# Optimization experiments

Measured on AMD Instinct MI355X. Metric: run time of the kernel, lower is better.

The kernel has to match this reference:

```python
import jax, jax.numpy as jnp
import numpy as np

# Object condensation loss config (matches init_kwargs / HGCalML defaults)
Q_MIN = 0.5
S_B = 1.0
POT_SCALE = 1.0
REP_SCALE = 1.0
BETA_SCALE = 1.0
E_WEIGHT = 1.0
HUBER_DELTA = 2.0
E_DEN_OFFSET = 1.0
K_MAX = 192          # object-id slots per event; id 0 = noise
EPS = 1e-6

B, N = 4, 50000


def setup_inputs() -> dict:
    key = jax.random.key(0)
    k1, k2, k3, k4, k5 = jax.random.split(key, 5)
    return {
        "beta": jax.random.uniform(k1, (B, N, 1), dtype=jnp.float32),
        "ccoords": jax.random.normal(k2, (B, N, 2), dtype=jnp.float32),
        "pred_energy": jax.random.uniform(k3, (B, N, 1), dtype=jnp.float32),
        "true_energy": jax.random.uniform(k4, (B, N, 1), dtype=jnp.float32),
        "truth_idx": jax.random.randint(k5, (B, N), 0, K_MAX, dtype=jnp.int32),
    }


def _per_event(beta, ccoords, pred_e, true_e, tidx):
    # beta: [N,1], ccoords: [N,2], tidx: [N] int (0 = noise)
    beta = jnp.clip(beta[:, 0], 1e-4, 1.0 - 1e-4)            # [N]
    q = jnp.arctanh(beta) ** 2 + Q_MIN                        # charge  [N]

    ids = jnp.arange(K_MAX)
    M = (tidx[:, None] == ids[None, :]) & (ids[None, :] > 0)  # [N,K] membership
    Mf = M.astype(q.dtype)
    obj_valid = jnp.any(M, axis=0)                            # [K]
    vf = obj_valid.astype(q.dtype)

    # condensation point alpha_k = argmax_q over members of object k
    qM = jnp.where(M, q[:, None], -1.0)                       # [N,K]
    idx_alpha = jnp.argmax(qM, axis=0)                        # [K]
    x_alpha = ccoords[idx_alpha]                              # [K,2]
    q_alpha = q[idx_alpha]                                    # [K]
    beta_alpha = beta[idx_alpha]                              # [K]

    # pairwise hit<->condensation-point distances
    d2 = jnp.sum((ccoords[:, None, :] - x_alpha[None, :, :]) ** 2, axis=-1)  # [N,K]

    # attractive potential (members), repulsive hinge (non-members of valid objects)
    att = jnp.sum(d2 * q_alpha[None, :] * Mf, axis=-1)                       # [N]
    dist = jnp.sqrt(d2 + EPS)
    rep = jnp.sum(jnp.maximum(0.0, 1.0 - dist) * q_alpha[None, :]
                  * (1.0 - Mf) * vf[None, :], axis=-1)                       # [N]
    L_V = jnp.mean(q * (POT_SCALE * att + REP_SCALE * rep))

    n_obj = jnp.sum(vf) + EPS
    L_beta = BETA_SCALE * jnp.sum((1.0 - beta_alpha) * vf) / n_obj

    noise = (tidx == 0).astype(q.dtype)
    L_noise = S_B * jnp.sum(beta * noise) / (jnp.sum(noise) + EPS)

    # energy payload loss: relative error, Huber, beta-weighted per object
    ediff = (pred_e[:, 0] - true_e[:, 0]) / (true_e[:, 0] + E_DEN_OFFSET)
    ad = jnp.abs(ediff)
    eh = jnp.where(ad <= HUBER_DELTA, 0.5 * ad ** 2,
                   HUBER_DELTA * (ad - 0.5 * HUBER_DELTA))                   # [N]
    pw = Mf * beta[:, None]                                                  # [N,K]
    per_obj_e = jnp.sum(pw * eh[:, None], axis=0) / (jnp.sum(pw, axis=0) + EPS)
    L_E = E_WEIGHT * jnp.sum(per_obj_e * vf) / n_obj

    return L_V + L_beta + L_noise + L_E


def reference(beta, ccoords, pred_energy, true_energy, truth_idx):
    per_ev = jax.vmap(_per_event)(beta, ccoords, pred_energy, true_energy, truth_idx)
    return jnp.mean(per_ev)
```

## Files before the change

### kernel.cpp

```cpp
#include <hip/hip_runtime.h>
#include <math.h>

#define KM 192
#define EPSF 1e-6f
#define QMIN 0.5f
#define BLKA 256
#define HA 4
#define TILEA (BLKA * HA)
#define BLKM 512

__device__ __forceinline__ float clipb(float b) {
    return fminf(fmaxf(b, 1e-4f), 1.0f - 1e-4f);
}
__device__ __forceinline__ float fast_atanh(float b) {
    float r = (1.f + b) * __builtin_amdgcn_rcpf(1.f - b);
    return 0.34657359f * __builtin_amdgcn_logf(r);
}

__global__ void __launch_bounds__(BLKA)
k_amax(const float* __restrict__ beta, const int* __restrict__ tidx,
       unsigned long long* __restrict__ pscr, int N, int HBT) {
    const int e = blockIdx.y;
    __shared__ unsigned long long smax[KM];
    for (int k = threadIdx.x; k < KM; k += BLKA) smax[k] = 0ull;
    __syncthreads();
    const size_t base = (size_t)e * N;
    #pragma unroll
    for (int h = 0; h < HA; ++h) {
        int i = blockIdx.x * TILEA + h * BLKA + threadIdx.x;
        if (i < N) {
            int t = tidx[base + i];
            if (t > 0) {
                float bc = clipb(beta[base + i]);
                unsigned long long pack =
                    ((unsigned long long)__float_as_uint(bc) << 32) |
                    (unsigned long long)(unsigned)(N - 1 - i);
                atomicMax(&smax[t], pack);
            }
        }
    }
    __syncthreads();
    unsigned long long* row = pscr + ((size_t)e * HBT + blockIdx.x) * KM;
    for (int k = threadIdx.x; k < KM; k += BLKA) row[k] = smax[k];
}

__global__ void __launch_bounds__(256)
k_alpha(const unsigned long long* __restrict__ pscr, const float* __restrict__ cc,
        float4* __restrict__ alpha, float* __restrict__ abw,
        float* __restrict__ enm, float* __restrict__ eden,
        float* __restrict__ scal, unsigned int* __restrict__ cnt,
        int N, int HBT) {
    const int e = blockIdx.x;
    const int k = threadIdx.x;
    if (k < KM) {
        const unsigned long long* pk = pscr + (size_t)e * HBT * KM + k;
        unsigned long long v = 0ull;
        #pragma unroll 8
        for (int t = 0; t < HBT; ++t) {
            unsigned long long p = pk[(size_t)t * KM];
            if (p > v) v = p;
        }
        float4 a = make_float4(0.f, 0.f, 0.f, EPSF);
        float bw = 0.f;
        if (v) {
            int idx = N - 1 - (int)(unsigned)(v & 0xffffffffull);
            bw = __uint_as_float((unsigned)(v >> 32));
            float at = fast_atanh(bw);
            float2 cp = ((const float2*)cc)[(size_t)e * N + idx];
            a.x = cp.x; a.y = cp.y;
            a.z = fmaf(at, at, QMIN);
            a.w = fmaf(cp.x, cp.x, fmaf(cp.y, cp.y, EPSF));
        }
        alpha[e * KM + k] = a;
        abw  [e * KM + k] = bw;
    }
    for (int z = threadIdx.x; z < KM; z += 256) {
        enm [e * KM + z] = 0.f;
        eden[e * KM + z] = 0.f;
    }
    if (threadIdx.x < 8) scal[e * 8 + threadIdx.x] = 0.f;
    if (blockIdx.x == 0 && threadIdx.x == 0) cnt[0] = 0u;
}

__global__ void __launch_bounds__(BLKM)
k_main(const float* __restrict__ beta, const float* __restrict__ cc,
       const float* __restrict__ pe,   const float* __restrict__ te,
       const int* __restrict__ tidx,   const float4* __restrict__ alpha,
       const float* __restrict__ abw,
       float* __restrict__ enm, float* __restrict__ eden,
       float* __restrict__ scal, unsigned int* __restrict__ cnt,
       float* __restrict__ out, int N, int B) {
    const int e = blockIdx.y;
    __shared__ float sn[KM], sd[KM];
    __shared__ float sw[24];
    __shared__ int   lastFlag;
    for (int k = threadIdx.x; k < KM; k += BLKM) { sn[k] = 0.f; sd[k] = 0.f; }
    __syncthreads();

    const size_t base = (size_t)e * N;
    const int i = blockIdx.x * BLKM + threadIdx.x;
    const bool ok = i < N;
    const size_t ii = base + (ok ? i : 0);
    float2 cp = ((const float2*)cc)[ii];
    float  bc = clipb(beta[ii]);
    int    t  = ok ? tidx[ii] : 0;
    float  at = fast_atanh(bc);
    float  qq = ok ? fmaf(at, at, QMIN) : 0.f;
    float  pp = fmaf(cp.x, cp.x, cp.y * cp.y);

    const float4* __restrict__ ae = alpha + e * KM;
    float r0 = 0.f, r1 = 0.f, r2 = 0.f, r3 = 0.f;
    for (int k = 0; k < KM; k += 4) {
        float4 a0 = ae[k], a1 = ae[k + 1], a2 = ae[k + 2], a3 = ae[k + 3];
        float d0 = fmaf(-2.f, fmaf(cp.x, a0.x, cp.y * a0.y), pp + a0.w);
        float d1 = fmaf(-2.f, fmaf(cp.x, a1.x, cp.y * a1.y), pp + a1.w);
        float d2 = fmaf(-2.f, fmaf(cp.x, a2.x, cp.y * a2.y), pp + a2.w);
        float d3 = fmaf(-2.f, fmaf(cp.x, a3.x, cp.y * a3.y), pp + a3.w);
        r0 = fmaf(fmaxf(1.f - __builtin_amdgcn_sqrtf(d0), 0.f), a0.z, r0);
        r1 = fmaf(fmaxf(1.f - __builtin_amdgcn_sqrtf(d1), 0.f), a1.z, r1);
        r2 = fmaf(fmaxf(1.f - __builtin_amdgcn_sqrtf(d2), 0.f), a2.z, r2);
        r3 = fmaf(fmaxf(1.f - __builtin_amdgcn_sqrtf(d3), 0.f), a3.z, r3);
    }
    float rep = (r0 + r1) + (r2 + r3);
    float att = 0.f, lv = 0.f, bn = 0.f, cn = 0.f;

    if (t > 0) {
        float4 av = ae[t];
        float dx = cp.x - av.x, dy = cp.y - av.y;
        float d2 = fmaf(dx, dx, dy * dy);
        att = d2 * av.z;
        rep -= fmaxf(1.f - __builtin_amdgcn_sqrtf(d2 + EPSF), 0.f) * av.z;
        float tev = te[ii];
        float edv = (pe[ii] - tev) * __builtin_amdgcn_rcpf(tev + 1.f);
        float ad  = fabsf(edv);
        float eh  = (ad <= 2.f) ? 0.5f * ad * ad : 2.f * (ad - 1.f);
        atomicAdd(&sn[t], bc * eh);
        atomicAdd(&sd[t], bc);
    } else if (ok) { bn = bc; cn = 1.f; }
    lv = qq * (att + rep);
    __syncthreads();

    if (threadIdx.x < KM) {
        float vd = sd[threadIdx.x];
        if (vd != 0.f) {
            atomicAdd(&enm [e * KM + threadIdx.x], sn[threadIdx.x]);
            atomicAdd(&eden[e * KM + threadIdx.x], vd);
        }
    }
    for (int off = 32; off > 0; off >>= 1) {
        lv += __shfl_down(lv, off);
        bn += __shfl_down(bn, off);
        cn += __shfl_down(cn, off);
    }
    const int wid = threadIdx.x >> 6;
    if ((threadIdx.x & 63) == 0) { sw[wid] = lv; sw[8 + wid] = bn; sw[16 + wid] = cn; }
    __syncthreads();
    if (threadIdx.x == 0) {
        float a = 0.f, b2 = 0.f, c2 = 0.f;
        #pragma unroll
        for (int w = 0; w < 8; ++w) { a += sw[w]; b2 += sw[8 + w]; c2 += sw[16 + w]; }
        atomicAdd(&scal[e * 8 + 0], a);
        atomicAdd(&scal[e * 8 + 3], b2);
        atomicAdd(&scal[e * 8 + 4], c2);
    }

    if (threadIdx.x == 0) {
        __threadfence();
        unsigned int old = atomicAdd(cnt, 1u);
        lastFlag = (old == gridDim.x * gridDim.y - 1u);
    }
    __syncthreads();
    if (!lastFlag) return;
    __threadfence();

    volatile float* ven = enm;
    volatile float* ved = eden;
    volatile float* vsc = scal;
    float tot = 0.f;
    for (int ev = 0; ev < B; ++ev) {
        float lb = 0.f, nv = 0.f, le = 0.f;
        if (threadIdx.x < KM) {
            float bw = abw[ev * KM + threadIdx.x];
            if (bw > 0.f) {
                lb = 1.f - bw;
                nv = 1.f;
                le = ven[ev * KM + threadIdx.x] / (ved[ev * KM + threadIdx.x] + EPSF);
            }
        }
        for (int off = 32; off > 0; off >>= 1) {
            lb += __shfl_down(lb, off);
            nv += __shfl_down(nv, off);
            le += __shfl_down(le, off);
        }
        if ((threadIdx.x & 63) == 0) { sw[wid] = lb; sw[8 + wid] = nv; sw[16 + wid] = le; }
        __syncthreads();
        if (threadIdx.x == 0) {
            float lbs = 0.f, nvs = 0.f, les = 0.f;
            #pragma unroll
            for (int w = 0; w < 8; ++w) { lbs += sw[w]; nvs += sw[8 + w]; les += sw[16 + w]; }
            float nobj = nvs + EPSF;
            tot += vsc[ev * 8 + 0] / (float)N + lbs / nobj
                 + vsc[ev * 8 + 3] / (vsc[ev * 8 + 4] + EPSF) + les / nobj;
        }
        __syncthreads();
    }
    if (threadIdx.x == 0) out[0] = tot / (float)B;
}

extern "C" void kernel_launch(void* const* d_in, const int* in_sizes, int n_in,
                              void* d_out, int out_size, void* d_ws, size_t ws_size,
                              hipStream_t stream) {
    const int B = 4;
    const int N = in_sizes[0] / B;
    const int HBT = (N + TILEA - 1) / TILEA;
    const int MB  = (N + BLKM - 1) / BLKM;

    const float* beta = (const float*)d_in[0];
    const float* cc   = (const float*)d_in[1];
    const float* pe   = (const float*)d_in[2];
    const float* te   = (const float*)d_in[3];
    const int*   tidx = (const int*)  d_in[4];
    float* out = (float*)d_out;

    char* ws = (char*)d_ws;
    unsigned long long* pscr = (unsigned long long*)ws;
    float4* alpha = (float4*)(ws + (size_t)B * HBT * KM * 8);
    float*  abw   = (float*)(alpha + B * KM);
    float*  enm   = abw  + B * KM;
    float*  eden  = enm  + B * KM;
    float*  scal  = eden + B * KM;
    unsigned int* cnt = (unsigned int*)(scal + B * 8);

    k_amax<<<dim3(HBT, B), dim3(BLKA), 0, stream>>>(beta, tidx, pscr, N, HBT);
    k_alpha<<<dim3(B), dim3(256), 0, stream>>>(pscr, cc, alpha, abw, enm, eden, scal, cnt, N, HBT);
    k_main<<<dim3(MB, B), dim3(BLKM), 0, stream>>>(
        beta, cc, pe, te, tidx, alpha, abw, enm, eden, scal, cnt, out, N, B);
}
```

Baseline: 98.99 us.

## Fuse argmax reduction via global atomics and last-block finalize, pack alphas in LDS

Merges the per-tile argmax scratch pass and the separate alpha-gather kernel into one kernel. Each block folds its maxima into global packed slots with atomicMax, and the last block to finish builds a SoA-packed alpha table. k_main now stages that table in shared memory and computes distances directly as dx²+dy² instead of the expanded form. Block size drops to 256. Workspace zeroing moves to a hipMemsetAsync, so there are still three stream operations but one fewer kernel and less scratch traffic; the cost is more global atomics from many more blocks.

```diff
diff --git a/kernel.cpp b/kernel.cpp
--- a/kernel.cpp
+++ b/kernel.cpp
@@ -2,12 +2,10 @@
 #include <math.h>
 
 #define KM 192
+#define KG 48
 #define EPSF 1e-6f
 #define QMIN 0.5f
-#define BLKA 256
-#define HA 4
-#define TILEA (BLKA * HA)
-#define BLKM 512
+#define BLK 256
 
 __device__ __forceinline__ float clipb(float b) {
     return fminf(fmaxf(b, 1e-4f), 1.0f - 1e-4f);
@@ -17,119 +15,122 @@
     return 0.34657359f * __builtin_amdgcn_logf(r);
 }
 
-__global__ void __launch_bounds__(BLKA)
+__global__ void __launch_bounds__(BLK)
 k_amax(const float* __restrict__ beta, const int* __restrict__ tidx,
-       unsigned long long* __restrict__ pscr, int N, int HBT) {
+       const float* __restrict__ cc,
+       unsigned long long* __restrict__ packs,
+       float* __restrict__ pkf, float* __restrict__ abw,
+       unsigned int* __restrict__ cnt, int N, int B) {
     const int e = blockIdx.y;
     __shared__ unsigned long long smax[KM];
-    for (int k = threadIdx.x; k < KM; k += BLKA) smax[k] = 0ull;
-    __syncthreads();
-    const size_t base = (size_t)e * N;
-    #pragma unroll
-    for (int h = 0; h < HA; ++h) {
-        int i = blockIdx.x * TILEA + h * BLKA + threadIdx.x;
-        if (i < N) {
-            int t = tidx[base + i];
-            if (t > 0) {
-                float bc = clipb(beta[base + i]);
-                unsigned long long pack =
-                    ((unsigned long long)__float_as_uint(bc) << 32) |
-                    (unsigned long long)(unsigned)(N - 1 - i);
-                atomicMax(&smax[t], pack);
-            }
-        }
-    }
-    __syncthreads();
-    unsigned long long* row = pscr + ((size_t)e * HBT + blockIdx.x) * KM;
-    for (int k = threadIdx.x; k < KM; k += BLKA) row[k] = smax[k];
-}
-
-__global__ void __launch_bounds__(256)
-k_alpha(const unsigned long long* __restrict__ pscr, const float* __restrict__ cc,
-        float4* __restrict__ alpha, float* __restrict__ abw,
-        float* __restrict__ enm, float* __restrict__ eden,
-        float* __restrict__ scal, unsigned int* __restrict__ cnt,
-        int N, int HBT) {
-    const int e = blockIdx.x;
-    const int k = threadIdx.x;
-    if (k < KM) {
-        const unsigned long long* pk = pscr + (size_t)e * HBT * KM + k;
-        unsigned long long v = 0ull;
-        #pragma unroll 8
-        for (int t = 0; t < HBT; ++t) {
-            unsigned long long p = pk[(size_t)t * KM];
-            if (p > v) v = p;
-        }
-        float4 a = make_float4(0.f, 0.f, 0.f, EPSF);
-        float bw = 0.f;
+    __shared__ int lastFlag;
+    if (threadIdx.x < KM) smax[threadIdx.x] = 0ull;
+    __syncthreads();
+    const int i = blockIdx.x * BLK + threadIdx.x;
+    if (i < N) {
+        int t = tidx[(size_t)e * N + i];
+        if (t > 0) {
+            float bc = clipb(beta[(size_t)e * N + i]);
+            unsigned long long pack =
+                ((unsigned long long)__float_as_uint(bc) << 32) |
+                (unsigned long long)(unsigned)(N - 1 - i);
+            atomicMax(&smax[t], pack);
+        }
+    }
+    __syncthreads();
+    if (threadIdx.x < KM) {
+        unsigned long long v = smax[threadIdx.x];
+        if (v) atomicMax(&packs[e * KM + threadIdx.x], v);
+    }
+
+    if (threadIdx.x == 0) {
+        __threadfence();
+        unsigned int old = atomicAdd(&cnt[0], 1u);
+        lastFlag = (old == gridDim.x * gridDim.y - 1u);
+    }
+    __syncthreads();
+    if (!lastFlag) return;
+
+    for (int s = threadIdx.x; s < B * KM; s += BLK) {
+        unsigned long long v = atomicMax(&packs[s], 0ull);
+        int e2 = s / KM, k = s - e2 * KM;
+        float x = 0.f, y = 0.f, q = 0.f, bw = 0.f;
         if (v) {
             int idx = N - 1 - (int)(unsigned)(v & 0xffffffffull);
             bw = __uint_as_float((unsigned)(v >> 32));
             float at = fast_atanh(bw);
-            float2 cp = ((const float2*)cc)[(size_t)e * N + idx];
-            a.x = cp.x; a.y = cp.y;
-            a.z = fmaf(at, at, QMIN);
-            a.w = fmaf(cp.x, cp.x, fmaf(cp.y, cp.y, EPSF));
-        }
-        alpha[e * KM + k] = a;
-        abw  [e * KM + k] = bw;
-    }
-    for (int z = threadIdx.x; z < KM; z += 256) {
-        enm [e * KM + z] = 0.f;
-        eden[e * KM + z] = 0.f;
-    }
-    if (threadIdx.x < 8) scal[e * 8 + threadIdx.x] = 0.f;
-    if (blockIdx.x == 0 && threadIdx.x == 0) cnt[0] = 0u;
-}
-
-__global__ void __launch_bounds__(BLKM)
+            q = fmaf(at, at, QMIN);
+            const float2 cp = ((const float2*)cc)[(size_t)e2 * N + idx];
+            x = cp.x; y = cp.y;
+        }
+        int g = k >> 2, m = k & 3;
+        float* basep = pkf + (size_t)(e2 * KG + g) * 12;
+        basep[(m >> 1) * 4 + (m & 1) * 2 + 0] = x;
+        basep[(m >> 1) * 4 + (m & 1) * 2 + 1] = y;
+        basep[8 + m] = q;
+        abw[s] = bw;
+    }
+}
+
+__global__ void __launch_bounds__(BLK)
 k_main(const float* __restrict__ beta, const float* __restrict__ cc,
        const float* __restrict__ pe,   const float* __restrict__ te,
-       const int* __restrict__ tidx,   const float4* __restrict__ alpha,
+       const int* __restrict__ tidx,   const float4* __restrict__ pk4,
        const float* __restrict__ abw,
        float* __restrict__ enm, float* __restrict__ eden,
        float* __restrict__ scal, unsigned int* __restrict__ cnt,
        float* __restrict__ out, int N, int B) {
     const int e = blockIdx.y;
-    __shared__ float sn[KM], sd[KM];
-    __shared__ float sw[24];
-    __shared__ int   lastFlag;
-    for (int k = threadIdx.x; k < KM; k += BLKM) { sn[k] = 0.f; sd[k] = 0.f; }
+    __shared__ float4 sa4[KG * 3];
+    __shared__ float  sn[KM], sd[KM];
+    __shared__ float  sw[12];
+    __shared__ int    lastFlag;
+    if (threadIdx.x < KG * 3) sa4[threadIdx.x] = pk4[e * KG * 3 + threadIdx.x];
+    if (threadIdx.x < KM) { sn[threadIdx.x] = 0.f; sd[threadIdx.x] = 0.f; }
     __syncthreads();
 
     const size_t base = (size_t)e * N;
-    const int i = blockIdx.x * BLKM + threadIdx.x;
+    const int i = blockIdx.x * BLK + threadIdx.x;
     const bool ok = i < N;
     const size_t ii = base + (ok ? i : 0);
-    float2 cp = ((const float2*)cc)[ii];
-    float  bc = clipb(beta[ii]);
-    int    t  = ok ? tidx[ii] : 0;
-    float  at = fast_atanh(bc);
-    float  qq = ok ? fmaf(at, at, QMIN) : 0.f;
-    float  pp = fmaf(cp.x, cp.x, cp.y * cp.y);
-
-    const float4* __restrict__ ae = alpha + e * KM;
+    const float2 cp = ((const float2*)cc)[ii];
+    const float  bc = clipb(beta[ii]);
+    const int    t  = ok ? tidx[ii] : 0;
+    const float  at = fast_atanh(bc);
+    const float  qq = ok ? fmaf(at, at, QMIN) : 0.f;
+
     float r0 = 0.f, r1 = 0.f, r2 = 0.f, r3 = 0.f;
-    for (int k = 0; k < KM; k += 4) {
-        float4 a0 = ae[k], a1 = ae[k + 1], a2 = ae[k + 2], a3 = ae[k + 3];
-        float d0 = fmaf(-2.f, fmaf(cp.x, a0.x, cp.y * a0.y), pp + a0.w);
-        float d1 = fmaf(-2.f, fmaf(cp.x, a1.x, cp.y * a1.y), pp + a1.w);
-        float d2 = fmaf(-2.f, fmaf(cp.x, a2.x, cp.y * a2.y), pp + a2.w);
-        float d3 = fmaf(-2.f, fmaf(cp.x, a3.x, cp.y * a3.y), pp + a3.w);
-        r0 = fmaf(fmaxf(1.f - __builtin_amdgcn_sqrtf(d0), 0.f), a0.z, r0);
-        r1 = fmaf(fmaxf(1.f - __builtin_amdgcn_sqrtf(d1), 0.f), a1.z, r1);
-        r2 = fmaf(fmaxf(1.f - __builtin_amdgcn_sqrtf(d2), 0.f), a2.z, r2);
-        r3 = fmaf(fmaxf(1.f - __builtin_amdgcn_sqrtf(d3), 0.f), a3.z, r3);
+    #pragma unroll 8
+    for (int g = 0; g < KG; ++g) {
+        float4 xy01 = sa4[g * 3 + 0];
+        float4 xy23 = sa4[g * 3 + 1];
+        float4 q4   = sa4[g * 3 + 2];
+        float dx0 = cp.x - xy01.x, dy0 = cp.y - xy01.y;
+        float dx1 = cp.x - xy01.z, dy1 = cp.y - xy01.w;
+        float dx2 = cp.x - xy23.x, dy2 = cp.y - xy23.y;
+        float dx3 = cp.x - xy23.z, dy3 = cp.y - xy23.w;
+        float d0 = fmaf(dx0, dx0, fmaf(dy0, dy0, EPSF));
+        float d1 = fmaf(dx1, dx1, fmaf(dy1, dy1, EPSF));
+        float d2 = fmaf(dx2, dx2, fmaf(dy2, dy2, EPSF));
+        float d3 = fmaf(dx3, dx3, fmaf(dy3, dy3, EPSF));
+        r0 = fmaf(fmaxf(1.f - __builtin_amdgcn_sqrtf(d0), 0.f), q4.x, r0);
+        r1 = fmaf(fmaxf(1.f - __builtin_amdgcn_sqrtf(d1), 0.f), q4.y, r1);
+        r2 = fmaf(fmaxf(1.f - __builtin_amdgcn_sqrtf(d2), 0.f), q4.z, r2);
+        r3 = fmaf(fmaxf(1.f - __builtin_amdgcn_sqrtf(d3), 0.f), q4.w, r3);
     }
     float rep = (r0 + r1) + (r2 + r3);
-    float att = 0.f, lv = 0.f, bn = 0.f, cn = 0.f;
+    float att = 0.f, bn = 0.f, cn = 0.f;
 
     if (t > 0) {
-        float4 av = ae[t];
-        float dx = cp.x - av.x, dy = cp.y - av.y;
+        const float* sf = (const float*)sa4;
+        int g = t >> 2, m = t & 3;
+        float xo = sf[g * 12 + (m >> 1) * 4 + (m & 1) * 2 + 0];
+        float yo = sf[g * 12 + (m >> 1) * 4 + (m & 1) * 2 + 1];
+        float qo = sf[g * 12 + 8 + m];
+        float dx = cp.x - xo, dy = cp.y - yo;
         float d2 = fmaf(dx, dx, dy * dy);
-        att = d2 * av.z;
-        rep -= fmaxf(1.f - __builtin_amdgcn_sqrtf(d2 + EPSF), 0.f) * av.z;
+        att = d2 * qo;
+        rep -= fmaxf(1.f - __builtin_amdgcn_sqrtf(d2 + EPSF), 0.f) * qo;
         float tev = te[ii];
         float edv = (pe[ii] - tev) * __builtin_amdgcn_rcpf(tev + 1.f);
         float ad  = fabsf(edv);
@@ -137,7 +138,7 @@
         atomicAdd(&sn[t], bc * eh);
         atomicAdd(&sd[t], bc);
     } else if (ok) { bn = bc; cn = 1.f; }
-    lv = qq * (att + rep);
+    float lv = qq * (att + rep);
     __syncthreads();
 
     if (threadIdx.x < KM) {
@@ -153,20 +154,17 @@
         cn += __shfl_down(cn, off);
     }
     const int wid = threadIdx.x >> 6;
-    if ((threadIdx.x & 63) == 0) { sw[wid] = lv; sw[8 + wid] = bn; sw[16 + wid] = cn; }
+    if ((threadIdx.x & 63) == 0) { sw[wid] = lv; sw[4 + wid] = bn; sw[8 + wid] = cn; }
     __syncthreads();
     if (threadIdx.x == 0) {
-        float a = 0.f, b2 = 0.f, c2 = 0.f;
-        #pragma unroll
-        for (int w = 0; w < 8; ++w) { a += sw[w]; b2 += sw[8 + w]; c2 += sw[16 + w]; }
-        atomicAdd(&scal[e * 8 + 0], a);
-        atomicAdd(&scal[e * 8 + 3], b2);
-        atomicAdd(&scal[e * 8 + 4], c2);
+        atomicAdd(&scal[e * 8 + 0], (sw[0] + sw[1]) + (sw[2] + sw[3]));
+        atomicAdd(&scal[e * 8 + 3], (sw[4] + sw[5]) + (sw[6] + sw[7]));
+        atomicAdd(&scal[e * 8 + 4], (sw[8] + sw[9]) + (sw[10] + sw[11]));
     }
 
     if (threadIdx.x == 0) {
         __threadfence();
-        unsigned int old = atomicAdd(cnt, 1u);
+        unsigned int old = atomicAdd(&cnt[1], 1u);
         lastFlag = (old == gridDim.x * gridDim.y - 1u);
     }
     __syncthreads();
@@ -192,12 +190,12 @@
             nv += __shfl_down(nv, off);
             le += __shfl_down(le, off);
         }
-        if ((threadIdx.x & 63) == 0) { sw[wid] = lb; sw[8 + wid] = nv; sw[16 + wid] = le; }
+        if ((threadIdx.x & 63) == 0) { sw[wid] = lb; sw[4 + wid] = nv; sw[8 + wid] = le; }
         __syncthreads();
         if (threadIdx.x == 0) {
-            float lbs = 0.f, nvs = 0.f, les = 0.f;
-            #pragma unroll
-            for (int w = 0; w < 8; ++w) { lbs += sw[w]; nvs += sw[8 + w]; les += sw[16 + w]; }
+            float lbs = (sw[0] + sw[1]) + (sw[2] + sw[3]);
+            float nvs = (sw[4] + sw[5]) + (sw[6] + sw[7]);
+            float les = (sw[8] + sw[9]) + (sw[10] + sw[11]);
             float nobj = nvs + EPSF;
             tot += vsc[ev * 8 + 0] / (float)N + lbs / nobj
                  + vsc[ev * 8 + 3] / (vsc[ev * 8 + 4] + EPSF) + les / nobj;
@@ -212,8 +210,7 @@
                               hipStream_t stream) {
     const int B = 4;
     const int N = in_sizes[0] / B;
-    const int HBT = (N + TILEA - 1) / TILEA;
-    const int MB  = (N + BLKM - 1) / BLKM;
+    const int MB = (N + BLK - 1) / BLK;
 
     const float* beta = (const float*)d_in[0];
     const float* cc   = (const float*)d_in[1];
@@ -223,16 +220,18 @@
     float* out = (float*)d_out;
 
     char* ws = (char*)d_ws;
-    unsigned long long* pscr = (unsigned long long*)ws;
-    float4* alpha = (float4*)(ws + (size_t)B * HBT * KM * 8);
-    float*  abw   = (float*)(alpha + B * KM);
-    float*  enm   = abw  + B * KM;
-    float*  eden  = enm  + B * KM;
-    float*  scal  = eden + B * KM;
+    unsigned long long* packs = (unsigned long long*)ws;
+    float4* pk4 = (float4*)(ws + (size_t)B * KM * 8);
+    float*  pkf = (float*)pk4;
+    float*  abw = (float*)(pk4 + B * KG * 3);
+    float*  enm = abw + B * KM;
+    float*  eden = enm + B * KM;
+    float*  scal = eden + B * KM;
     unsigned int* cnt = (unsigned int*)(scal + B * 8);
-
-    k_amax<<<dim3(HBT, B), dim3(BLKA), 0, stream>>>(beta, tidx, pscr, N, HBT);
-    k_alpha<<<dim3(B), dim3(256), 0, stream>>>(pscr, cc, alpha, abw, enm, eden, scal, cnt, N, HBT);
-    k_main<<<dim3(MB, B), dim3(BLKM), 0, stream>>>(
-        beta, cc, pe, te, tidx, alpha, abw, enm, eden, scal, cnt, out, N, B);
-}
+    const size_t zeroBytes = (char*)(cnt + 4) - ws;
+
+    (void)hipMemsetAsync(d_ws, 0, zeroBytes, stream);
+    k_amax<<<dim3(MB, B), dim3(BLK), 0, stream>>>(beta, tidx, cc, packs, pkf, abw, cnt, N, B);
+    k_main<<<dim3(MB, B), dim3(BLK), 0, stream>>>(
+        beta, cc, pe, te, tidx, pk4, abw, enm, eden, scal, cnt, out, N, B);
+}
```

New measurement: 121.5 us. +22.7%, slower.

## Process two hits per thread in main kernel and move final reduction to separate kernel

Applied to the files above, without the earlier changes.

Each thread in the main kernel now handles two hits, so every alpha float4 load from memory is shared across two distance computations. The block size drops to 256 and launch bounds request more occupancy. The distance is now computed directly as dx²+dy²+eps instead of the expanded dot-product form with a precomputed norm. The last-block-done counter and threadfence finalization are replaced by a separate single-block finalize kernel, which removes the global atomic counter but adds a launch.

```diff
diff --git a/kernel.cpp b/kernel.cpp
--- a/kernel.cpp
+++ b/kernel.cpp
@@ -7,7 +7,8 @@
 #define BLKA 256
 #define HA 4
 #define TILEA (BLKA * HA)
-#define BLKM 512
+#define BLKM 256
+#define TILEM (BLKM * 2)
 
 __device__ __forceinline__ float clipb(float b) {
     return fminf(fmaxf(b, 1e-4f), 1.0f - 1e-4f);
@@ -48,8 +49,7 @@
 k_alpha(const unsigned long long* __restrict__ pscr, const float* __restrict__ cc,
         float4* __restrict__ alpha, float* __restrict__ abw,
         float* __restrict__ enm, float* __restrict__ eden,
-        float* __restrict__ scal, unsigned int* __restrict__ cnt,
-        int N, int HBT) {
+        float* __restrict__ scal, int N, int HBT) {
     const int e = blockIdx.x;
     const int k = threadIdx.x;
     if (k < KM) {
@@ -60,7 +60,7 @@
             unsigned long long p = pk[(size_t)t * KM];
             if (p > v) v = p;
         }
-        float4 a = make_float4(0.f, 0.f, 0.f, EPSF);
+        float4 a = make_float4(0.f, 0.f, 0.f, 0.f);
         float bw = 0.f;
         if (v) {
             int idx = N - 1 - (int)(unsigned)(v & 0xffffffffull);
@@ -69,7 +69,6 @@
             float2 cp = ((const float2*)cc)[(size_t)e * N + idx];
             a.x = cp.x; a.y = cp.y;
             a.z = fmaf(at, at, QMIN);
-            a.w = fmaf(cp.x, cp.x, fmaf(cp.y, cp.y, EPSF));
         }
         alpha[e * KM + k] = a;
         abw  [e * KM + k] = bw;
@@ -79,65 +78,87 @@
         eden[e * KM + z] = 0.f;
     }
     if (threadIdx.x < 8) scal[e * 8 + threadIdx.x] = 0.f;
-    if (blockIdx.x == 0 && threadIdx.x == 0) cnt[0] = 0u;
-}
-
-__global__ void __launch_bounds__(BLKM)
+}
+
+__global__ void __launch_bounds__(BLKM, 4)
 k_main(const float* __restrict__ beta, const float* __restrict__ cc,
        const float* __restrict__ pe,   const float* __restrict__ te,
        const int* __restrict__ tidx,   const float4* __restrict__ alpha,
-       const float* __restrict__ abw,
        float* __restrict__ enm, float* __restrict__ eden,
-       float* __restrict__ scal, unsigned int* __restrict__ cnt,
-       float* __restrict__ out, int N, int B) {
+       float* __restrict__ scal, int N) {
     const int e = blockIdx.y;
     __shared__ float sn[KM], sd[KM];
-    __shared__ float sw[24];
-    __shared__ int   lastFlag;
+    __shared__ float sw[12];
     for (int k = threadIdx.x; k < KM; k += BLKM) { sn[k] = 0.f; sd[k] = 0.f; }
     __syncthreads();
 
     const size_t base = (size_t)e * N;
-    const int i = blockIdx.x * BLKM + threadIdx.x;
-    const bool ok = i < N;
-    const size_t ii = base + (ok ? i : 0);
-    float2 cp = ((const float2*)cc)[ii];
-    float  bc = clipb(beta[ii]);
-    int    t  = ok ? tidx[ii] : 0;
-    float  at = fast_atanh(bc);
-    float  qq = ok ? fmaf(at, at, QMIN) : 0.f;
-    float  pp = fmaf(cp.x, cp.x, cp.y * cp.y);
+    const int ia = blockIdx.x * TILEM + threadIdx.x;
+    const int ib = ia + BLKM;
+    const bool oka = ia < N, okb = ib < N;
+    const size_t iia = base + (oka ? ia : 0);
+    const size_t iib = base + (okb ? ib : 0);
+    const float2 ca = ((const float2*)cc)[iia];
+    const float2 cb = ((const float2*)cc)[iib];
+    const float bca = clipb(beta[iia]);
+    const float bcb = clipb(beta[iib]);
+    const int   ta  = oka ? tidx[iia] : 0;
+    const int   tb  = okb ? tidx[iib] : 0;
+    const float ha_ = fast_atanh(bca);
+    const float hb_ = fast_atanh(bcb);
+    const float qa  = oka ? fmaf(ha_, ha_, QMIN) : 0.f;
+    const float qb  = okb ? fmaf(hb_, hb_, QMIN) : 0.f;
 
     const float4* __restrict__ ae = alpha + e * KM;
-    float r0 = 0.f, r1 = 0.f, r2 = 0.f, r3 = 0.f;
-    for (int k = 0; k < KM; k += 4) {
-        float4 a0 = ae[k], a1 = ae[k + 1], a2 = ae[k + 2], a3 = ae[k + 3];
-        float d0 = fmaf(-2.f, fmaf(cp.x, a0.x, cp.y * a0.y), pp + a0.w);
-        float d1 = fmaf(-2.f, fmaf(cp.x, a1.x, cp.y * a1.y), pp + a1.w);
-        float d2 = fmaf(-2.f, fmaf(cp.x, a2.x, cp.y * a2.y), pp + a2.w);
-        float d3 = fmaf(-2.f, fmaf(cp.x, a3.x, cp.y * a3.y), pp + a3.w);
-        r0 = fmaf(fmaxf(1.f - __builtin_amdgcn_sqrtf(d0), 0.f), a0.z, r0);
-        r1 = fmaf(fmaxf(1.f - __builtin_amdgcn_sqrtf(d1), 0.f), a1.z, r1);
-        r2 = fmaf(fmaxf(1.f - __builtin_amdgcn_sqrtf(d2), 0.f), a2.z, r2);
-        r3 = fmaf(fmaxf(1.f - __builtin_amdgcn_sqrtf(d3), 0.f), a3.z, r3);
-    }
-    float rep = (r0 + r1) + (r2 + r3);
-    float att = 0.f, lv = 0.f, bn = 0.f, cn = 0.f;
-
-    if (t > 0) {
-        float4 av = ae[t];
-        float dx = cp.x - av.x, dy = cp.y - av.y;
+    float ra0 = 0.f, ra1 = 0.f, rb0 = 0.f, rb1 = 0.f;
+    #pragma unroll 8
+    for (int k = 0; k < KM; k += 2) {
+        float4 a0 = ae[k], a1 = ae[k + 1];
+        float dxa0 = ca.x - a0.x, dya0 = ca.y - a0.y;
+        float dxa1 = ca.x - a1.x, dya1 = ca.y - a1.y;
+        float dxb0 = cb.x - a0.x, dyb0 = cb.y - a0.y;
+        float dxb1 = cb.x - a1.x, dyb1 = cb.y - a1.y;
+        float da0 = fmaf(dxa0, dxa0, fmaf(dya0, dya0, EPSF));
+        float da1 = fmaf(dxa1, dxa1, fmaf(dya1, dya1, EPSF));
+        float db0 = fmaf(dxb0, dxb0, fmaf(dyb0, dyb0, EPSF));
+        float db1 = fmaf(dxb1, dxb1, fmaf(dyb1, dyb1, EPSF));
+        ra0 = fmaf(fmaxf(1.f - __builtin_amdgcn_sqrtf(da0), 0.f), a0.z, ra0);
+        ra1 = fmaf(fmaxf(1.f - __builtin_amdgcn_sqrtf(da1), 0.f), a1.z, ra1);
+        rb0 = fmaf(fmaxf(1.f - __builtin_amdgcn_sqrtf(db0), 0.f), a0.z, rb0);
+        rb1 = fmaf(fmaxf(1.f - __builtin_amdgcn_sqrtf(db1), 0.f), a1.z, rb1);
+    }
+    float repa = ra0 + ra1, repb = rb0 + rb1;
+    float atta = 0.f, attb = 0.f, bn = 0.f, cn = 0.f;
+
+    if (ta > 0) {
+        float4 av = ae[ta];
+        float dx = ca.x - av.x, dy = ca.y - av.y;
         float d2 = fmaf(dx, dx, dy * dy);
-        att = d2 * av.z;
-        rep -= fmaxf(1.f - __builtin_amdgcn_sqrtf(d2 + EPSF), 0.f) * av.z;
-        float tev = te[ii];
-        float edv = (pe[ii] - tev) * __builtin_amdgcn_rcpf(tev + 1.f);
+        atta = d2 * av.z;
+        repa -= fmaxf(1.f - __builtin_amdgcn_sqrtf(d2 + EPSF), 0.f) * av.z;
+        float tev = te[iia];
+        float edv = (pe[iia] - tev) * __builtin_amdgcn_rcpf(tev + 1.f);
         float ad  = fabsf(edv);
         float eh  = (ad <= 2.f) ? 0.5f * ad * ad : 2.f * (ad - 1.f);
-        atomicAdd(&sn[t], bc * eh);
-        atomicAdd(&sd[t], bc);
-    } else if (ok) { bn = bc; cn = 1.f; }
-    lv = qq * (att + rep);
+        atomicAdd(&sn[ta], bca * eh);
+        atomicAdd(&sd[ta], bca);
+    } else if (oka) { bn += bca; cn += 1.f; }
+
+    if (tb > 0) {
+        float4 av = ae[tb];
+        float dx = cb.x - av.x, dy = cb.y - av.y;
+        float d2 = fmaf(dx, dx, dy * dy);
+        attb = d2 * av.z;
+        repb -= fmaxf(1.f - __builtin_amdgcn_sqrtf(d2 + EPSF), 0.f) * av.z;
+        float tev = te[iib];
+        float edv = (pe[iib] - tev) * __builtin_amdgcn_rcpf(tev + 1.f);
+        float ad  = fabsf(edv);
+        float eh  = (ad <= 2.f) ? 0.5f * ad * ad : 2.f * (ad - 1.f);
+        atomicAdd(&sn[tb], bcb * eh);
+        atomicAdd(&sd[tb], bcb);
+    } else if (okb) { bn += bcb; cn += 1.f; }
+
+    float lv = fmaf(qa, atta + repa, qb * (attb + repb));
     __syncthreads();
 
     if (threadIdx.x < KM) {
@@ -153,29 +174,21 @@
         cn += __shfl_down(cn, off);
     }
     const int wid = threadIdx.x >> 6;
-    if ((threadIdx.x & 63) == 0) { sw[wid] = lv; sw[8 + wid] = bn; sw[16 + wid] = cn; }
+    if ((threadIdx.x & 63) == 0) { sw[wid] = lv; sw[4 + wid] = bn; sw[8 + wid] = cn; }
     __syncthreads();
     if (threadIdx.x == 0) {
-        float a = 0.f, b2 = 0.f, c2 = 0.f;
-        #pragma unroll
-        for (int w = 0; w < 8; ++w) { a += sw[w]; b2 += sw[8 + w]; c2 += sw[16 + w]; }
-        atomicAdd(&scal[e * 8 + 0], a);
-        atomicAdd(&scal[e * 8 + 3], b2);
-        atomicAdd(&scal[e * 8 + 4], c2);
-    }
-
-    if (threadIdx.x == 0) {
-        __threadfence();
-        unsigned int old = atomicAdd(cnt, 1u);
-        lastFlag = (old == gridDim.x * gridDim.y - 1u);
-    }
-    __syncthreads();
-    if (!lastFlag) return;
-    __threadfence();
-
-    volatile float* ven = enm;
-    volatile float* ved = eden;
-    volatile float* vsc = scal;
+        atomicAdd(&scal[e * 8 + 0], (sw[0] + sw[1]) + (sw[2] + sw[3]));
+        atomicAdd(&scal[e * 8 + 3], (sw[4] + sw[5]) + (sw[6] + sw[7]));
+        atomicAdd(&scal[e * 8 + 4], (sw[8] + sw[9]) + (sw[10] + sw[11]));
+    }
+}
+
+__global__ void __launch_bounds__(256)
+k_fin(const float* __restrict__ enm, const float* __restrict__ eden,
+      const float* __restrict__ abw, const float* __restrict__ scal,
+      float* __restrict__ out, int N, int B) {
+    __shared__ float sred[12];
+    const int wid = threadIdx.x >> 6;
     float tot = 0.f;
     for (int ev = 0; ev < B; ++ev) {
         float lb = 0.f, nv = 0.f, le = 0.f;
@@ -184,7 +197,7 @@
             if (bw > 0.f) {
                 lb = 1.f - bw;
                 nv = 1.f;
-                le = ven[ev * KM + threadIdx.x] / (ved[ev * KM + threadIdx.x] + EPSF);
+                le = enm[ev * KM + threadIdx.x] / (eden[ev * KM + threadIdx.x] + EPSF);
             }
         }
         for (int off = 32; off > 0; off >>= 1) {
@@ -192,15 +205,15 @@
             nv += __shfl_down(nv, off);
             le += __shfl_down(le, off);
         }
-        if ((threadIdx.x & 63) == 0) { sw[wid] = lb; sw[8 + wid] = nv; sw[16 + wid] = le; }
+        if ((threadIdx.x & 63) == 0) { sred[wid] = lb; sred[4 + wid] = nv; sred[8 + wid] = le; }
         __syncthreads();
         if (threadIdx.x == 0) {
-            float lbs = 0.f, nvs = 0.f, les = 0.f;
-            #pragma unroll
-            for (int w = 0; w < 8; ++w) { lbs += sw[w]; nvs += sw[8 + w]; les += sw[16 + w]; }
+            float lbs = (sred[0] + sred[1]) + (sred[2] + sred[3]);
+            float nvs = (sred[4] + sred[5]) + (sred[6] + sred[7]);
+            float les = (sred[8] + sred[9]) + (sred[10] + sred[11]);
             float nobj = nvs + EPSF;
-            tot += vsc[ev * 8 + 0] / (float)N + lbs / nobj
-                 + vsc[ev * 8 + 3] / (vsc[ev * 8 + 4] + EPSF) + les / nobj;
+            tot += scal[ev * 8 + 0] / (float)N + lbs / nobj
+                 + scal[ev * 8 + 3] / (scal[ev * 8 + 4] + EPSF) + les / nobj;
         }
         __syncthreads();
     }
@@ -213,7 +226,7 @@
     const int B = 4;
     const int N = in_sizes[0] / B;
     const int HBT = (N + TILEA - 1) / TILEA;
-    const int MB  = (N + BLKM - 1) / BLKM;
+    const int MB  = (N + TILEM - 1) / TILEM;
 
     const float* beta = (const float*)d_in[0];
     const float* cc   = (const float*)d_in[1];
@@ -229,10 +242,10 @@
     float*  enm   = abw  + B * KM;
     float*  eden  = enm  + B * KM;
     float*  scal  = eden + B * KM;
-    unsigned int* cnt = (unsigned int*)(scal + B * 8);
 
     k_amax<<<dim3(HBT, B), dim3(BLKA), 0, stream>>>(beta, tidx, pscr, N, HBT);
-    k_alpha<<<dim3(B), dim3(256), 0, stream>>>(pscr, cc, alpha, abw, enm, eden, scal, cnt, N, HBT);
+    k_alpha<<<dim3(B), dim3(256), 0, stream>>>(pscr, cc, alpha, abw, enm, eden, scal, N, HBT);
     k_main<<<dim3(MB, B), dim3(BLKM), 0, stream>>>(
-        beta, cc, pe, te, tidx, alpha, abw, enm, eden, scal, cnt, out, N, B);
-}
+        beta, cc, pe, te, tidx, alpha, enm, eden, scal, N);
+    k_fin<<<dim3(1), dim3(256), 0, stream>>>(enm, eden, abw, scal, out, N, B);
+}
```

Result: no change. 99.99 us (+1.0%).
